# Kernel optimization log

Hardware: AMD Instinct MI355X
Metric: run time of the kernel (lower is better)

## Reference

```python
import jax, jax.numpy as jnp
import numpy as np

D, U, NNZ, B = 8192, 4096, 1_700_000, 1024

def setup_inputs() -> dict:
    key = jax.random.key(0)
    k1, k2, k3, k4 = jax.random.split(key, 4)
    x = jax.random.normal(k1, (B, D), dtype=jnp.float32)
    kernel_vector = jax.random.normal(k2, (NNZ,), dtype=jnp.float32) * 0.02
    bias = jax.random.normal(k3, (U,), dtype=jnp.float32) * 0.01
    flat = jax.random.randint(k4, (NNZ,), 0, D * U)  # random sparsity pattern
    nonzero_ind = jnp.stack([flat // U, flat % U], axis=1).astype(jnp.int32)  # [NNZ, 2]
    return {"x": x, "kernel_vector": kernel_vector, "bias": bias, "nonzero_ind": nonzero_ind}

def reference(x, kernel_vector, bias, nonzero_ind):
    # scatter_nd: build dense (D, U) kernel from nonzero entries (duplicates add, as in tf.scatter_nd)
    W = jnp.zeros((D, U), dtype=kernel_vector.dtype).at[nonzero_ind[:, 0], nonzero_ind[:, 1]].add(kernel_vector)
    out = x @ W + bias  # [B, U]
    return jnp.tanh(out)
```

## Files before the change

### kernel.cpp

```cpp
#include <hip/hip_runtime.h>
#include <hip/hip_fp16.h>
#include <cmath>

#define DIM_M 1024
#define DIM_K 8192
#define DIM_N 4096
#define SPLIT 4
#define KSPL  (DIM_K / SPLIT)
#define BKT   32
#define NTT   (KSPL / BKT)
#define NB    1024
#define EPB   8192

typedef __attribute__((ext_vector_type(8))) _Float16 half8;
typedef __attribute__((ext_vector_type(4))) float floatx4;

struct __align__(8) Half4 { __half2 a, b; };

__device__ inline void gload_lds16(const void* g, void* l) {
    __builtin_amdgcn_global_load_lds(
        (const __attribute__((address_space(1))) void*)g,
        (__attribute__((address_space(3))) void*)l, 16, 0, 0);
}

__global__ void cvt_f2h(const floatx4* __restrict__ in, Half4* __restrict__ out, int n4) {
    int i = blockIdx.x * blockDim.x + threadIdx.x;
    if (i < n4) {
        floatx4 f = in[i];
        Half4 h;
        h.a = __floats2half2_rn(f.x, f.y);
        h.b = __floats2half2_rn(f.z, f.w);
        out[i] = h;
    }
}


__global__ __launch_bounds__(512) void hist_k(const int* __restrict__ ind,
                                              unsigned* __restrict__ cnt, int nnz) {
    __shared__ unsigned h[NB];
    const int tid = threadIdx.x;
    for (int i = tid; i < NB; i += 512) h[i] = 0u;
    __syncthreads();
    const int base = blockIdx.x * EPB;
    const int lim = min(nnz - base, EPB);
    const int4* ip = (const int4*)(ind + 2 * (size_t)base);
    for (int k2 = tid; k2 < lim / 2; k2 += 512) {
        int4 w = ip[k2];
        atomicAdd(&h[w.y >> 2], 1u);
        atomicAdd(&h[w.w >> 2], 1u);
    }
    if ((lim & 1) && tid == 0) {
        int u = ind[2 * (size_t)(base + lim - 1) + 1];
        atomicAdd(&h[u >> 2], 1u);
    }
    __syncthreads();
    for (int i = tid; i < NB; i += 512) cnt[(size_t)blockIdx.x * NB + i] = h[i];
}

__global__ void scanb_k(unsigned* cnt, unsigned* __restrict__ bb, int nblk) {
    __shared__ unsigned s[256];
    const int tid = threadIdx.x, bin = blockIdx.x;
    unsigned carry = 0;
    for (int c0 = 0; c0 < nblk; c0 += 256) {
        int b = c0 + tid;
        unsigned v = (b < nblk) ? cnt[(size_t)b * NB + bin] : 0u;
        s[tid] = v;
        __syncthreads();
        for (int off = 1; off < 256; off <<= 1) {
            unsigned add = (tid >= off) ? s[tid - off] : 0u;
            __syncthreads();
            s[tid] += add;
            __syncthreads();
        }
        if (b < nblk) cnt[(size_t)b * NB + bin] = carry + s[tid] - v;
        carry += s[255];
        __syncthreads();
    }
    if (tid == 0) bb[bin] = carry;
}

__global__ void scant_k(unsigned* bb) {
    __shared__ unsigned s[NB];
    const int tid = threadIdx.x;
    unsigned v = bb[tid];
    s[tid] = v;
    __syncthreads();
    for (int off = 1; off < NB; off <<= 1) {
        unsigned add = (tid >= off) ? s[tid - off] : 0u;
        __syncthreads();
        s[tid] += add;
        __syncthreads();
    }
    bb[tid] = s[tid] - v;
    if (tid == NB - 1) bb[NB] = s[tid];
}

__global__ __launch_bounds__(512) void reorder_k(const int* __restrict__ ind,
                                                 const float* __restrict__ kv,
                                                 const unsigned* __restrict__ start,
                                                 const unsigned* __restrict__ bb,
                                                 uint2* __restrict__ ebuf, int nnz) {
    extern __shared__ char rsm[];
    uint2*    buf  = (uint2*)rsm;
    unsigned* gofs = (unsigned*)(rsm + 65536);
    unsigned* cur  = (unsigned*)(rsm + 98304);
    unsigned* dl   = (unsigned*)(rsm + 102400);
    unsigned* ss   = (unsigned*)(rsm + 106496);
    const int tid = threadIdx.x, blk = blockIdx.x;
    const int base = blk * EPB;
    const int lim = min(nnz - base, EPB);
    const int4*   ip = (const int4*)(ind + 2 * (size_t)base);
    const float2* vp = (const float2*)(kv + base);

    for (int i = tid; i < NB; i += 512) cur[i] = 0u;
    __syncthreads();
    for (int k2 = tid; k2 < lim / 2; k2 += 512) {
        int4 w = ip[k2];
        atomicAdd(&cur[w.y >> 2], 1u);
        atomicAdd(&cur[w.w >> 2], 1u);
    }
    if ((lim & 1) && tid == 0) {
        int u = ind[2 * (size_t)(base + lim - 1) + 1];
        atomicAdd(&cur[u >> 2], 1u);
    }
    __syncthreads();
    unsigned c0 = cur[2 * tid], c1 = cur[2 * tid + 1];
    unsigned own = c0 + c1;
    ss[tid] = own;
    __syncthreads();
    for (int off = 1; off < 512; off <<= 1) {
        unsigned t = (tid >= off) ? ss[tid - off] : 0u;
        __syncthreads();
        ss[tid] += t;
        __syncthreads();
    }
    unsigned e0 = ss[tid] - own;
    unsigned e1 = e0 + c0;
    __syncthreads();
    cur[2 * tid]     = e0;
    cur[2 * tid + 1] = e1;
    unsigned g0 = bb[2 * tid]     + start[(size_t)blk * NB + 2 * tid];
    unsigned g1 = bb[2 * tid + 1] + start[(size_t)blk * NB + 2 * tid + 1];
    dl[2 * tid]     = g0 - e0;
    dl[2 * tid + 1] = g1 - e1;
    __syncthreads();
    for (int k2 = tid; k2 < lim / 2; k2 += 512) {
        int4 w = ip[k2];
        float2 v = vp[k2];
        int b0 = w.y >> 2, b1 = w.w >> 2;
        unsigned r0 = atomicAdd(&cur[b0], 1u);
        buf[r0]  = make_uint2(((unsigned)(w.y & 3) << 13) | (unsigned)w.x, __float_as_uint(v.x));
        gofs[r0] = dl[b0] + r0;
        unsigned r1 = atomicAdd(&cur[b1], 1u);
        buf[r1]  = make_uint2(((unsigned)(w.w & 3) << 13) | (unsigned)w.z, __float_as_uint(v.y));
        gofs[r1] = dl[b1] + r1;
    }
    if ((lim & 1) && tid == 0) {
        size_t e = (size_t)base + lim - 1;
        int d = ind[2 * e], u = ind[2 * e + 1];
        int b = u >> 2;
        unsigned r = atomicAdd(&cur[b], 1u);
        buf[r]  = make_uint2(((unsigned)(u & 3) << 13) | (unsigned)d, __float_as_uint(kv[e]));
        gofs[r] = dl[b] + r;
    }
    __syncthreads();
    for (int j = tid; j < lim; j += 512)
        ebuf[gofs[j]] = buf[j];
}

__global__ __launch_bounds__(512) void accum_k(const uint2* __restrict__ ebuf,
                                               const unsigned* __restrict__ bb,
                                               Half4* __restrict__ wh4) {
    extern __shared__ float reg[];
    floatx4* reg4 = (floatx4*)reg;
    const int tid = threadIdx.x, bin = blockIdx.x;
    for (int i = tid; i < 8192; i += 512) reg4[i] = floatx4{0.f, 0.f, 0.f, 0.f};
    __syncthreads();
    const unsigned s0 = bb[bin], s1 = bb[bin + 1];
    for (unsigned e = s0 + tid; e < s1; e += 512) {
        uint2 p = ebuf[e];
        atomicAdd(&reg[p.x], __uint_as_float(p.y));
    }
    __syncthreads();
    for (int i = tid; i < 8192; i += 512) {
        floatx4 f = reg4[i];
        Half4 h;
        h.a = __floats2half2_rn(f.x, f.y);
        h.b = __floats2half2_rn(f.z, f.w);
        wh4[(size_t)bin * 8192 + i] = h;
    }
}

__global__ __launch_bounds__(512, 2) void gemm8_k(
    const _Float16* __restrict__ Ah,
    const _Float16* __restrict__ Bh,
    _Float16*       __restrict__ part)
{
    extern __shared__ char smem[];

    const int tid  = threadIdx.x;
    const int lane = tid & 63;
    const int wave = tid >> 6;

    const int bid = blockIdx.x;
    const int swz = (bid & 7) * 32 + (bid >> 3);
    const int n0  = (swz >> 4) * 256;
    const int rem = swz & 15;
    const int m0  = (rem >> 2) * 256;
    const int sp  = rem & 3;
    const size_t kbase = (size_t)sp * KSPL;

    const int srow = tid >> 2;
    const int sch  = (tid & 3) ^ ((tid >> 3) & 3);
    const _Float16* aSg = Ah + (size_t)(m0 + srow) * DIM_K + kbase + sch * 8;
    const _Float16* bSg = Bh + (size_t)(n0 + srow) * DIM_K + kbase + sch * 8;
    const int wofs = wave * 1024;

    const int wrm = wave >> 2;
    const int wn  = wave & 3;
    const int q   = lane >> 4;
    const char* aRd = smem + (wrm * 128 + (lane & 15)) * 64;
    const char* bRd = smem + 16384 + (wn * 64 + (lane & 15)) * 64;
    const int ch = (q ^ ((lane >> 1) & 3)) * 16;

    floatx4 acc[8][4] = {};
    half8 aF[4], bF[4];

#define STA(SB)                                                               \
    { gload_lds16(aSg,                         smem + (SB) * 32768 + wofs);   \
      gload_lds16(aSg + (size_t)128 * DIM_K,   smem + (SB) * 32768 + 8192 + wofs); }
#define STB(SB)                                                               \
    { gload_lds16(bSg,                         smem + (SB) * 32768 + 16384 + wofs); \
      gload_lds16(bSg + (size_t)128 * DIM_K,   smem + (SB) * 32768 + 24576 + wofs); }
#define ADV() { aSg += BKT; bSg += BKT; }

#define PH0(CB, SB)                                                           \
    { _Pragma("unroll") for (int i = 0; i < 4; ++i)                           \
        aF[i] = *(const half8*)(aRd + (CB) * 32768 + i * 1024 + ch);          \
      _Pragma("unroll") for (int i = 0; i < 4; ++i)                           \
        bF[i] = *(const half8*)(bRd + (CB) * 32768 + i * 1024 + ch);          \
      STA(SB)                                                                 \
      __builtin_amdgcn_s_barrier();                                           \
      asm volatile("s_waitcnt lgkmcnt(0)" ::: "memory");                      \
      __builtin_amdgcn_sched_barrier(0);                                      \
      __builtin_amdgcn_s_setprio(1);                                          \
      _Pragma("unroll") for (int mi = 0; mi < 4; ++mi)                        \
        _Pragma("unroll") for (int ni = 0; ni < 4; ++ni)                      \
          acc[mi][ni] = __builtin_amdgcn_mfma_f32_16x16x32_f16(               \
              aF[mi], bF[ni], acc[mi][ni], 0, 0, 0);                          \
      __builtin_amdgcn_s_setprio(0);                                          \
      __builtin_amdgcn_s_barrier(); }

#define PH1(CB, SB)                                                           \
    { _Pragma("unroll") for (int i = 0; i < 4; ++i)                           \
        aF[i] = *(const half8*)(aRd + (CB) * 32768 + 4096 + i * 1024 + ch);   \
      STB(SB) ADV()                                                           \
      __builtin_amdgcn_s_barrier();                                           \
      asm volatile("s_waitcnt lgkmcnt(0)" ::: "memory");                      \
      __builtin_amdgcn_sched_barrier(0);                                      \
      __builtin_amdgcn_s_setprio(1);                                          \
      _Pragma("unroll") for (int mi = 0; mi < 4; ++mi)                        \
        _Pragma("unroll") for (int ni = 0; ni < 4; ++ni)                      \
          acc[4 + mi][ni] = __builtin_amdgcn_mfma_f32_16x16x32_f16(           \
              aF[mi], bF[ni], acc[4 + mi][ni], 0, 0, 0);                      \
      __builtin_amdgcn_s_setprio(0);                                          \
      asm volatile("s_waitcnt vmcnt(8)" ::: "memory");                        \
      __builtin_amdgcn_s_barrier(); }

#define KTILE(CB, SB) PH0(CB, SB) PH1(CB, SB)

    STA(0) STB(0) ADV()
    STA(1) STB(1) ADV()
    STA(2) STB(2) ADV()
    asm volatile("s_waitcnt vmcnt(8)" ::: "memory");
    __builtin_amdgcn_s_barrier();

    for (int it = 0; it < NTT / 4; ++it) {
        KTILE(0, 3)
        KTILE(1, 0)
        KTILE(2, 1)
        KTILE(3, 2)
    }

#undef KTILE
#undef PH1
#undef PH0
#undef ADV
#undef STB
#undef STA

    _Float16* pbase = part + (size_t)sp * DIM_M * DIM_N;
    #pragma unroll
    for (int ni = 0; ni < 4; ++ni) {
        const int col = n0 + wn * 64 + ni * 16 + (lane & 15);
        #pragma unroll
        for (int mi = 0; mi < 8; ++mi) {
            const int row = m0 + wrm * 128 + mi * 16 + (q << 2);
            #pragma unroll
            for (int r = 0; r < 4; ++r)
                pbase[(size_t)(row + r) * DIM_N + col] = (_Float16)acc[mi][ni][r];
        }
    }
}

__global__ void reduce_tanh(const Half4* __restrict__ part, const float* __restrict__ bias,
                            floatx4* __restrict__ out) {
    const int n4 = DIM_M * DIM_N / 4;
    int i = blockIdx.x * blockDim.x + threadIdx.x;
    if (i < n4) {
        float sx = 0.f, sy = 0.f, sz = 0.f, sw = 0.f;
        #pragma unroll
        for (int sp = 0; sp < SPLIT; ++sp) {
            Half4 p = part[(size_t)sp * n4 + i];
            float2 lo = __half22float2(p.a);
            float2 hi = __half22float2(p.b);
            sx += lo.x; sy += lo.y; sz += hi.x; sw += hi.y;
        }
        floatx4 b = ((const floatx4*)bias)[i & (DIM_N / 4 - 1)];
        floatx4 o;
        o.x = tanhf(sx + b.x);
        o.y = tanhf(sy + b.y);
        o.z = tanhf(sz + b.z);
        o.w = tanhf(sw + b.w);
        out[i] = o;
    }
}

extern "C" void kernel_launch(void* const* d_in, const int* in_sizes, int n_in,
                              void* d_out, int out_size, void* d_ws, size_t ws_size,
                              hipStream_t stream) {
    const float* x    = (const float*)d_in[0];
    const float* kv   = (const float*)d_in[1];
    const float* bias = (const float*)d_in[2];
    const int*   ind  = (const int*)d_in[3];
    float* out = (float*)d_out;
    const int nnz = in_sizes[1];

    char* ws = (char*)d_ws;
    _Float16* wh = (_Float16*)ws;
    const size_t whBytes = (size_t)DIM_N * DIM_K * 2;
    _Float16* xh = (_Float16*)(ws + whBytes);
    const size_t xhBytes = (size_t)DIM_M * DIM_K * 2;
    _Float16* part = (_Float16*)(ws + whBytes + xhBytes);
    const size_t partBytes = (size_t)SPLIT * DIM_M * DIM_N * 2;
    uint2* ebuf = (uint2*)(ws + whBytes + xhBytes + partBytes);
    const size_t ebufBytes = (size_t)16 << 20;
    unsigned* cnt = (unsigned*)(ws + whBytes + xhBytes + partBytes + ebufBytes);
    const size_t cntBytes = (size_t)1024 * NB * 4;
    unsigned* bb = (unsigned*)(ws + whBytes + xhBytes + partBytes + ebufBytes + cntBytes);

    const int xN4 = (int)((size_t)DIM_M * DIM_K / 4);
    const int oN4 = DIM_M * DIM_N / 4;
    const int nblk = (nnz + EPB - 1) / EPB;

    cvt_f2h<<<(xN4 + 255) / 256, 256, 0, stream>>>((const floatx4*)x, (Half4*)xh, xN4);
    hist_k<<<nblk, 512, 0, stream>>>(ind, cnt, nnz);
    scanb_k<<<NB, 256, 0, stream>>>(cnt, bb, nblk);
    scant_k<<<1, NB, 0, stream>>>(bb);

    hipFuncSetAttribute((const void*)reorder_k,
                        hipFuncAttributeMaxDynamicSharedMemorySize, 131072);
    reorder_k<<<nblk, 512, 110592, stream>>>(ind, kv, cnt, bb, ebuf, nnz);

    hipFuncSetAttribute((const void*)accum_k,
                        hipFuncAttributeMaxDynamicSharedMemorySize, 131072);
    accum_k<<<NB, 512, 131072, stream>>>(ebuf, bb, (Half4*)wh);

    hipFuncSetAttribute((const void*)gemm8_k,
                        hipFuncAttributeMaxDynamicSharedMemorySize, 131072);
    gemm8_k<<<dim3(256), 512, 131072, stream>>>(xh, wh, part);

    reduce_tanh<<<(oN4 + 255) / 256, 256, 0, stream>>>((const Half4*)part, bias, (floatx4*)out);
}
```

Before: 135.9 us.

## Double-buffer MFMA fragments in registers and use one barrier per k-tile

The GEMM main loop is rebuilt so each k-tile runs as one step instead of two half-phases. Each step prefetches the next tile's full A/B fragments from LDS into a second register set, issues the next global-to-LDS stage, then runs all 32 MFMAs on the current fragments. This replaces four barriers and two lgkmcnt stalls per tile with a single wait and barrier, so LDS reads can overlap the matrix math. The cost is more VGPRs for the doubled fragment arrays, which could lower occupancy or cause spills.

```diff
diff --git a/kernel.cpp b/kernel.cpp
--- a/kernel.cpp
+++ b/kernel.cpp
@@ -224,70 +224,56 @@
     const int ch = (q ^ ((lane >> 1) & 3)) * 16;
 
     floatx4 acc[8][4] = {};
-    half8 aF[4], bF[4];
-
-#define STA(SB)                                                               \
-    { gload_lds16(aSg,                         smem + (SB) * 32768 + wofs);   \
-      gload_lds16(aSg + (size_t)128 * DIM_K,   smem + (SB) * 32768 + 8192 + wofs); }
-#define STB(SB)                                                               \
-    { gload_lds16(bSg,                         smem + (SB) * 32768 + 16384 + wofs); \
-      gload_lds16(bSg + (size_t)128 * DIM_K,   smem + (SB) * 32768 + 24576 + wofs); }
-#define ADV() { aSg += BKT; bSg += BKT; }
-
-#define PH0(CB, SB)                                                           \
-    { _Pragma("unroll") for (int i = 0; i < 4; ++i)                           \
-        aF[i] = *(const half8*)(aRd + (CB) * 32768 + i * 1024 + ch);          \
+    half8 aF0[8], bF0[4], aF1[8], bF1[4];
+
+#define STAGE(SB)                                                             \
+    { gload_lds16(aSg,                       smem + (SB) * 32768 + wofs);     \
+      gload_lds16(aSg + (size_t)128 * DIM_K, smem + (SB) * 32768 + 8192 + wofs); \
+      gload_lds16(bSg,                       smem + (SB) * 32768 + 16384 + wofs); \
+      gload_lds16(bSg + (size_t)128 * DIM_K, smem + (SB) * 32768 + 24576 + wofs); \
+      aSg += BKT; bSg += BKT; }
+
+#define READF(RA, RB, CB)                                                     \
+    { _Pragma("unroll") for (int i = 0; i < 8; ++i)                           \
+        RA[i] = *(const half8*)(aRd + (CB) * 32768 + i * 1024 + ch);          \
       _Pragma("unroll") for (int i = 0; i < 4; ++i)                           \
-        bF[i] = *(const half8*)(bRd + (CB) * 32768 + i * 1024 + ch);          \
-      STA(SB)                                                                 \
-      __builtin_amdgcn_s_barrier();                                           \
-      asm volatile("s_waitcnt lgkmcnt(0)" ::: "memory");                      \
-      __builtin_amdgcn_sched_barrier(0);                                      \
-      __builtin_amdgcn_s_setprio(1);                                          \
-      _Pragma("unroll") for (int mi = 0; mi < 4; ++mi)                        \
+        RB[i] = *(const half8*)(bRd + (CB) * 32768 + i * 1024 + ch); }
+
+#define MM(RA, RB)                                                            \
+    { __builtin_amdgcn_s_setprio(1);                                         \
+      _Pragma("unroll") for (int mi = 0; mi < 8; ++mi)                        \
         _Pragma("unroll") for (int ni = 0; ni < 4; ++ni)                      \
           acc[mi][ni] = __builtin_amdgcn_mfma_f32_16x16x32_f16(               \
-              aF[mi], bF[ni], acc[mi][ni], 0, 0, 0);                          \
-      __builtin_amdgcn_s_setprio(0);                                          \
-      __builtin_amdgcn_s_barrier(); }
-
-#define PH1(CB, SB)                                                           \
-    { _Pragma("unroll") for (int i = 0; i < 4; ++i)                           \
-        aF[i] = *(const half8*)(aRd + (CB) * 32768 + 4096 + i * 1024 + ch);   \
-      STB(SB) ADV()                                                           \
-      __builtin_amdgcn_s_barrier();                                           \
-      asm volatile("s_waitcnt lgkmcnt(0)" ::: "memory");                      \
-      __builtin_amdgcn_sched_barrier(0);                                      \
-      __builtin_amdgcn_s_setprio(1);                                          \
-      _Pragma("unroll") for (int mi = 0; mi < 4; ++mi)                        \
-        _Pragma("unroll") for (int ni = 0; ni < 4; ++ni)                      \
-          acc[4 + mi][ni] = __builtin_amdgcn_mfma_f32_16x16x32_f16(           \
-              aF[mi], bF[ni], acc[4 + mi][ni], 0, 0, 0);                      \
-      __builtin_amdgcn_s_setprio(0);                                          \
-      asm volatile("s_waitcnt vmcnt(8)" ::: "memory");                        \
-      __builtin_amdgcn_s_barrier(); }
-
-#define KTILE(CB, SB) PH0(CB, SB) PH1(CB, SB)
-
-    STA(0) STB(0) ADV()
-    STA(1) STB(1) ADV()
-    STA(2) STB(2) ADV()
-    asm volatile("s_waitcnt vmcnt(8)" ::: "memory");
+              RA[mi], RB[ni], acc[mi][ni], 0, 0, 0);                          \
+      __builtin_amdgcn_s_setprio(0); }
+
+#define BODY(CBN, SB, AU, BU, AL, BL)                                         \
+    READF(AL, BL, CBN)                                                        \
+    STAGE(SB)                                                                 \
+    MM(AU, BU)                                                                \
+    asm volatile("s_waitcnt vmcnt(4) lgkmcnt(0)" ::: "memory");               \
+    __builtin_amdgcn_sched_barrier(0);                                        \
+    __builtin_amdgcn_s_barrier();                                             \
+    __builtin_amdgcn_sched_barrier(0);
+
+    STAGE(0) STAGE(1) STAGE(2)
+    asm volatile("s_waitcnt vmcnt(4)" ::: "memory");
     __builtin_amdgcn_s_barrier();
+    READF(aF0, bF0, 0)
+    asm volatile("s_waitcnt lgkmcnt(0)" ::: "memory");
+    __builtin_amdgcn_sched_barrier(0);
 
     for (int it = 0; it < NTT / 4; ++it) {
-        KTILE(0, 3)
-        KTILE(1, 0)
-        KTILE(2, 1)
-        KTILE(3, 2)
-    }
-
-#undef KTILE
-#undef PH1
-#undef PH0
-#undef ADV
-#undef STB
-#undef STA
+        BODY(1, 3, aF0, bF0, aF1, bF1)
+        BODY(2, 0, aF1, bF1, aF0, bF0)
+        BODY(3, 1, aF0, bF0, aF1, bF1)
+        BODY(0, 2, aF1, bF1, aF0, bF0)
+    }
+
+#undef BODY
+#undef MM
+#undef READF
+#undef STAGE
 
     _Float16* pbase = part + (size_t)sp * DIM_M * DIM_N;
     #pragma unroll
```

After: 156.7 us. 1.15x slower.
